# Optimization experiments

Measured on AMD Instinct MI355X. Metric: run time of the kernel, lower is better.

## Reference

```python
import jax, jax.numpy as jnp
import numpy as np

SEQ, BATCH, HID, OUT = 2048, 128, 256, 2

def setup_inputs() -> dict:
    key = jax.random.key(0)
    ks = jax.random.split(key, 8)
    x = jax.random.normal(ks[0], (SEQ, BATCH), dtype=jnp.float32)
    h0 = jax.random.normal(ks[1], (BATCH, HID), dtype=jnp.float32) * 0.1
    noise = jax.random.normal(ks[2], (SEQ, BATCH, HID), dtype=jnp.float32) * 0.1
    W_ih = jax.random.normal(ks[3], (HID, 1), dtype=jnp.float32) * 0.1 + 0.5
    W_hh = jax.random.normal(ks[4], (HID, HID), dtype=jnp.float32) * 0.4
    W_hh_bias = jax.random.normal(ks[5], (HID, HID), dtype=jnp.float32) * 0.1 + 0.1
    b_h = jnp.zeros((HID,), dtype=jnp.float32)
    W = jax.random.normal(ks[6], (OUT, HID), dtype=jnp.float32) * 0.3
    b = jnp.zeros((OUT,), dtype=jnp.float32)
    return dict(x=x, h0=h0, noise=noise, W_ih=W_ih, W_hh=W_hh,
                W_hh_bias=W_hh_bias, b_h=b_h, W=W, b=b, context=1)

def reference(x, h0, noise, W_ih, W_hh, W_hh_bias, b_h, W, b, context):
    # input_size == 1, so x_t @ W_ih.T is an outer product with W_ih[:, 0]
    w_in = W_ih[:, 0]                       # (hid,)
    # context is a scalar, so c1 transposes cancel: W_eff = W_hh + context*W_hh_bias
    W_eff = W_hh + context * W_hh_bias      # (hid, hid)

    def step(h, inp):
        x_t, n_t = inp                      # (batch,), (batch, hid)
        h = jnp.tanh(h @ W_eff.T + x_t[:, None] * w_in[None, :] + b_h) + n_t
        return h, h

    _, out = jax.lax.scan(step, h0, (x, noise))   # (seq, batch, hid)
    out = jnp.transpose(out, (1, 0, 2))           # (batch, seq, hid)
    y = jax.nn.sigmoid(jnp.einsum('bsh,oh->bso', out, W) + b)
    return y[:, :, 0], out
```

## Files before the change

kernel.cpp:

```cpp
#include <hip/hip_runtime.h>
#include <math.h>

#define SEQ   2048
#define BATCH 128
#define HID   256

#define DPP_XOR1  0xB1
#define DPP_XOR2  0x4E
#define DPP_XOR7  0x141
#define DPP_XOR15 0x140
template<int CTRL>
__device__ __forceinline__ float dppf(float v) {
    return __builtin_bit_cast(float, __builtin_amdgcn_update_dpp(
        0, __builtin_bit_cast(int, v), CTRL, 0xF, 0xF, true));
}

#define BARRIER() do { asm volatile("s_waitcnt lgkmcnt(0)" ::: "memory"); \
                       __builtin_amdgcn_s_barrier(); } while (0)

__global__ __launch_bounds__(512, 2) void rnn_kernel(
    const float* __restrict__ x,
    const float* __restrict__ h0,
    const float* __restrict__ noise,
    const float* __restrict__ W_ih,
    const float* __restrict__ W_hh,
    const float* __restrict__ W_hhb,
    const float* __restrict__ b_h,
    const float* __restrict__ Wy,
    const float* __restrict__ by,
    const int*   __restrict__ ctx,
    float* __restrict__ h_out,
    float* __restrict__ y_out)
{
    const int b    = blockIdx.x;
    const int tid  = threadIdx.x;
    const int w    = tid >> 6;
    const int lane = tid & 63;
    const int jg   = lane >> 3;
    const int kg   = lane & 7;
    const int j0   = w * 32 + jg * 4;
    const int jres = j0 + (kg & 3);

    __shared__ __align__(16) float hbuf[2][HID];
    __shared__ __align__(16) float ywave[2][32];

    int iv = *ctx;
    float c = (iv > 1000000 || iv < -1000000) ? __int_as_float(iv) : (float)iv;

    float wreg[4][32];
    #pragma unroll
    for (int e = 0; e < 4; ++e) {
        const float4* wr  = (const float4*)&W_hh [(j0 + e) * HID + kg * 32];
        const float4* wrb = (const float4*)&W_hhb[(j0 + e) * HID + kg * 32];
        #pragma unroll
        for (int q = 0; q < 8; ++q) {
            float4 av = wr[q], bv = wrb[q];
            wreg[e][4*q+0] = av.x + c * bv.x;
            wreg[e][4*q+1] = av.y + c * bv.y;
            wreg[e][4*q+2] = av.z + c * bv.z;
            wreg[e][4*q+3] = av.w + c * bv.w;
        }
    }

    const float win = W_ih[jres];
    const float bh  = b_h[jres];
    const float w0  = Wy[jres];
    const float b0v = by[0];

    if (tid < HID) {
        int cc = tid >> 5, ii = (tid >> 2) & 7, ee = tid & 3;
        hbuf[0][cc * 32 + (((ii + cc) & 7) << 2) + ee] = h0[b * HID + tid];
    }

    int voff[8];
    #pragma unroll
    for (int i = 0; i < 8; ++i)
        voff[i] = kg * 128 + (((i + kg) & 7) << 4);

    const int  b0k = kg & 1;
    const int  b1k = (kg >> 1) & 1;
    const bool wr4 = (kg < 4);
    const int  wslot = w * 32 + (((jg + w) & 7) << 2) + kg;

    float x_next  = x[b];
    float n_next  = noise[(size_t)b * HID + jres];
    float x_next2 = x[BATCH + b];
    float n_next2 = noise[((size_t)BATCH + b) * HID + jres];
    const float* xp = x + 2 * BATCH + b;
    const float* np = noise + ((size_t)2 * BATCH + b) * HID + jres;

    float* hop = h_out + (size_t)b * SEQ * HID;
    float* yp  = y_out + (size_t)b * SEQ;

    __syncthreads();

#define STEP(T, CUR)                                                         \
  {                                                                          \
    const float x_t = x_next;                                                \
    const float n_t = n_next;                                                \
    x_next = x_next2;  n_next = n_next2;                                     \
    x_next2 = *xp;     n_next2 = *np;                                        \
    if ((T) + 3 < SEQ) { xp += BATCH; np += (size_t)BATCH * HID; }           \
    const char* hb = (const char*)&hbuf[CUR][0];                             \
    float p0 = 0.f, p1 = 0.f, p2 = 0.f, p3 = 0.f;                            \
    _Pragma("unroll")                                                        \
    for (int i = 0; i < 8; ++i) {                                            \
      float4 h4 = *(const float4*)(hb + voff[i]);                            \
      p0 = fmaf(h4.x, wreg[0][4*i+0], p0);                                   \
      p0 = fmaf(h4.y, wreg[0][4*i+1], p0);                                   \
      p0 = fmaf(h4.z, wreg[0][4*i+2], p0);                                   \
      p0 = fmaf(h4.w, wreg[0][4*i+3], p0);                                   \
      p1 = fmaf(h4.x, wreg[1][4*i+0], p1);                                   \
      p1 = fmaf(h4.y, wreg[1][4*i+1], p1);                                   \
      p1 = fmaf(h4.z, wreg[1][4*i+2], p1);                                   \
      p1 = fmaf(h4.w, wreg[1][4*i+3], p1);                                   \
      p2 = fmaf(h4.x, wreg[2][4*i+0], p2);                                   \
      p2 = fmaf(h4.y, wreg[2][4*i+1], p2);                                   \
      p2 = fmaf(h4.z, wreg[2][4*i+2], p2);                                   \
      p2 = fmaf(h4.w, wreg[2][4*i+3], p2);                                   \
      p3 = fmaf(h4.x, wreg[3][4*i+0], p3);                                   \
      p3 = fmaf(h4.y, wreg[3][4*i+1], p3);                                   \
      p3 = fmaf(h4.z, wreg[3][4*i+2], p3);                                   \
      p3 = fmaf(h4.w, wreg[3][4*i+3], p3);                                   \
    }                                                                        \
     \
    if (w == ((T) & 7) && (T) > 0) {                                         \
      float4 yv = *(const float4*)&ywave[(CUR) ^ 1][(lane & 7) * 4];         \
      float s = (yv.x + yv.y) + (yv.z + yv.w);                               \
      s += dppf<DPP_XOR1>(s);                                                \
      s += dppf<DPP_XOR2>(s);                                                \
      s += dppf<DPP_XOR7>(s);                                                \
      if (lane == 0) yp[(T) - 1] = 1.f / (1.f + __expf(-(s + b0v)));         \
    }                                                                        \
    \
    \
    p0 += dppf<DPP_XOR7>(p0);                                                \
    p1 += dppf<DPP_XOR7>(p1);                                                \
    p2 += dppf<DPP_XOR7>(p2);                                                \
    p3 += dppf<DPP_XOR7>(p3);                                                \
    float m0 = b0k ? p1 : p0,  s0 = b0k ? p0 : p1;                           \
    float m1 = b0k ? p3 : p2,  s1 = b0k ? p2 : p3;                           \
    float q0 = m0 + dppf<DPP_XOR1>(s0);                                      \
    float q1 = m1 + dppf<DPP_XOR1>(s1);                                      \
    float mm = b1k ? q1 : q0,  ss = b1k ? q0 : q1;                           \
    float r  = mm + dppf<DPP_XOR2>(ss);                                      \
    float z  = fmaf(x_t, win, r) + bh;                                       \
    float ex = __expf(2.f * z);              \
    float hn = 1.f - 2.f / (ex + 1.f) + n_t;                                 \
    if (wr4) {                                                               \
      hbuf[(CUR) ^ 1][wslot] = hn;       \
      hop[jres] = hn;                                                        \
    }                                                                        \
    \
    float qy = wr4 ? hn * w0 : 0.f;                                          \
    qy += dppf<DPP_XOR1>(qy);                                                \
    qy += dppf<DPP_XOR2>(qy);                                                \
    qy += dppf<DPP_XOR7>(qy);                                                \
    qy += dppf<DPP_XOR15>(qy);                                               \
    if ((lane & 15) == 0) ywave[CUR][w * 4 + (lane >> 4)] = qy;              \
    hop += HID;                                                              \
    BARRIER();                                                               \
  }

    for (int t = 0; t < SEQ; t += 2) {
        STEP(t, 0)
        STEP(t + 1, 1)
    }

    if (w == 0) {
        float4 yv = *(const float4*)&ywave[1][(lane & 7) * 4];
        float s = (yv.x + yv.y) + (yv.z + yv.w);
        s += dppf<DPP_XOR1>(s);
        s += dppf<DPP_XOR2>(s);
        s += dppf<DPP_XOR7>(s);
        if (lane == 0) yp[SEQ - 1] = 1.f / (1.f + __expf(-(s + b0v)));
    }
#undef STEP
}

extern "C" void kernel_launch(void* const* d_in, const int* in_sizes, int n_in,
                              void* d_out, int out_size, void* d_ws, size_t ws_size,
                              hipStream_t stream) {
    const float* x     = (const float*)d_in[0];
    const float* h0    = (const float*)d_in[1];
    const float* noise = (const float*)d_in[2];
    const float* W_ih  = (const float*)d_in[3];
    const float* W_hh  = (const float*)d_in[4];
    const float* W_hhb = (const float*)d_in[5];
    const float* b_h   = (const float*)d_in[6];
    const float* W     = (const float*)d_in[7];
    const float* bvec  = (const float*)d_in[8];
    const int*   ctx   = (const int*)d_in[9];

    float* y_out = (float*)d_out;
    float* h_out = (float*)d_out + (size_t)BATCH * SEQ;

    rnn_kernel<<<dim3(BATCH), dim3(512), 0, stream>>>(
        x, h0, noise, W_ih, W_hh, W_hhb, b_h, W, bvec, ctx, h_out, y_out);
}
```

Measured before the change: 2.231 ms.

## Repartition recurrent matvec with packed FMA and defer output work off critical path

Each lane now owns 8 output rows by 16 k-values instead of 4 by 32, and the dot products use v_pk_fma_f32 on float2 pairs, halving FMA instruction count. The hidden-state LDS buffer uses a padded chunk layout so each lane reads four contiguous vec4s. The global h store and y-projection reduction for step t are deferred into step t+1 so they run off the tanh-to-barrier critical path. The tanh and sigmoid divisions now use approximate rcp. This adds more DPP reduction stages, a delayed finalisation sequence, and slightly lower precision.

```diff
diff --git a/kernel.cpp b/kernel.cpp
--- a/kernel.cpp
+++ b/kernel.cpp
@@ -4,6 +4,10 @@
 #define SEQ   2048
 #define BATCH 128
 #define HID   256
+#define CHUNK_B 80
+
+typedef float vf2 __attribute__((ext_vector_type(2)));
+typedef float vf4 __attribute__((ext_vector_type(4)));
 
 #define DPP_XOR1  0xB1
 #define DPP_XOR2  0x4E
@@ -14,6 +18,9 @@
     return __builtin_bit_cast(float, __builtin_amdgcn_update_dpp(
         0, __builtin_bit_cast(int, v), CTRL, 0xF, 0xF, true));
 }
+
+#define PKFMA(acc, a, b) \
+    asm("v_pk_fma_f32 %0, %1, %2, %0" : "+v"(acc) : "v"(a), "v"(b))
 
 #define BARRIER() do { asm volatile("s_waitcnt lgkmcnt(0)" ::: "memory"); \
                        __builtin_amdgcn_s_barrier(); } while (0)
@@ -36,29 +43,31 @@
     const int tid  = threadIdx.x;
     const int w    = tid >> 6;
     const int lane = tid & 63;
-    const int jg   = lane >> 3;
-    const int kg   = lane & 7;
-    const int j0   = w * 32 + jg * 4;
-    const int jres = j0 + (kg & 3);
-
-    __shared__ __align__(16) float hbuf[2][HID];
+    const int jg   = lane >> 4;
+    const int kg   = lane & 15;
+    const int j0   = w * 32 + jg * 8;
+    const int jres = j0 + (lane & 7);
+    const bool wr  = (lane & 8) == 0;
+
+    __shared__ __align__(16) char  hbuf[2][16 * CHUNK_B];
     __shared__ __align__(16) float ywave[2][32];
 
     int iv = *ctx;
     float c = (iv > 1000000 || iv < -1000000) ? __int_as_float(iv) : (float)iv;
 
-    float wreg[4][32];
+    vf2 wreg2[8][8];
     #pragma unroll
-    for (int e = 0; e < 4; ++e) {
-        const float4* wr  = (const float4*)&W_hh [(j0 + e) * HID + kg * 32];
-        const float4* wrb = (const float4*)&W_hhb[(j0 + e) * HID + kg * 32];
+    for (int e = 0; e < 8; ++e) {
+        const vf4* wrp  = (const vf4*)&W_hh [(j0 + e) * HID + kg * 16];
+        const vf4* wrbp = (const vf4*)&W_hhb[(j0 + e) * HID + kg * 16];
         #pragma unroll
-        for (int q = 0; q < 8; ++q) {
-            float4 av = wr[q], bv = wrb[q];
-            wreg[e][4*q+0] = av.x + c * bv.x;
-            wreg[e][4*q+1] = av.y + c * bv.y;
-            wreg[e][4*q+2] = av.z + c * bv.z;
-            wreg[e][4*q+3] = av.w + c * bv.w;
+        for (int q = 0; q < 4; ++q) {
+            vf4 av = wrp[q], bv = wrbp[q];
+            vf2 lo, hi;
+            lo.x = av.x + c * bv.x;  lo.y = av.y + c * bv.y;
+            hi.x = av.z + c * bv.z;  hi.y = av.w + c * bv.w;
+            wreg2[e][2 * q]     = lo;
+            wreg2[e][2 * q + 1] = hi;
         }
     }
 
@@ -67,20 +76,14 @@
     const float w0  = Wy[jres];
     const float b0v = by[0];
 
-    if (tid < HID) {
-        int cc = tid >> 5, ii = (tid >> 2) & 7, ee = tid & 3;
-        hbuf[0][cc * 32 + (((ii + cc) & 7) << 2) + ee] = h0[b * HID + tid];
-    }
-
-    int voff[8];
-    #pragma unroll
-    for (int i = 0; i < 8; ++i)
-        voff[i] = kg * 128 + (((i + kg) & 7) << 4);
-
-    const int  b0k = kg & 1;
-    const int  b1k = (kg >> 1) & 1;
-    const bool wr4 = (kg < 4);
-    const int  wslot = w * 32 + (((jg + w) & 7) << 2) + kg;
+    if (tid < HID)
+        *(float*)&hbuf[0][(tid >> 4) * CHUNK_B + (tid & 15) * 4] = h0[b * HID + tid];
+
+    const char* hrpA = &hbuf[0][kg * CHUNK_B];
+    const char* hrpB = &hbuf[1][kg * CHUNK_B];
+    const int   wbyte = (jres >> 4) * CHUNK_B + (jres & 15) * 4;
+    float* wpA = (float*)&hbuf[0][wbyte];
+    float* wpB = (float*)&hbuf[1][wbyte];
 
     float x_next  = x[b];
     float n_next  = noise[(size_t)b * HID + jres];
@@ -89,91 +92,127 @@
     const float* xp = x + 2 * BATCH + b;
     const float* np = noise + ((size_t)2 * BATCH + b) * HID + jres;
 
-    float* hop = h_out + (size_t)b * SEQ * HID;
-    float* yp  = y_out + (size_t)b * SEQ;
+    float* hout_b = h_out + (size_t)b * SEQ * HID;
+    float* yp     = y_out + (size_t)b * SEQ;
+    int    ho     = 0;
+    float  hn_prev = 0.f;
 
     __syncthreads();
 
-#define STEP(T, CUR)                                                         \
+#define STEP(HRP, WPT, DO_PREV, YWW, DO_FIN, YWR, FINW, TFIN, ADV)           \
   {                                                                          \
-    const float x_t = x_next;                                                \
-    const float n_t = n_next;                                                \
+                                          \
+    vf4 h40 = *(const vf4*)((HRP) + 0);                                      \
+    vf4 h41 = *(const vf4*)((HRP) + 16);                                     \
+    vf4 h42 = *(const vf4*)((HRP) + 32);                                     \
+    vf4 h43 = *(const vf4*)((HRP) + 48);                                     \
+    const float x_t = x_next, n_t = n_next;                                  \
     x_next = x_next2;  n_next = n_next2;                                     \
     x_next2 = *xp;     n_next2 = *np;                                        \
-    if ((T) + 3 < SEQ) { xp += BATCH; np += (size_t)BATCH * HID; }           \
-    const char* hb = (const char*)&hbuf[CUR][0];                             \
-    float p0 = 0.f, p1 = 0.f, p2 = 0.f, p3 = 0.f;                            \
-    _Pragma("unroll")                                                        \
-    for (int i = 0; i < 8; ++i) {                                            \
-      float4 h4 = *(const float4*)(hb + voff[i]);                            \
-      p0 = fmaf(h4.x, wreg[0][4*i+0], p0);                                   \
-      p0 = fmaf(h4.y, wreg[0][4*i+1], p0);                                   \
-      p0 = fmaf(h4.z, wreg[0][4*i+2], p0);                                   \
-      p0 = fmaf(h4.w, wreg[0][4*i+3], p0);                                   \
-      p1 = fmaf(h4.x, wreg[1][4*i+0], p1);                                   \
-      p1 = fmaf(h4.y, wreg[1][4*i+1], p1);                                   \
-      p1 = fmaf(h4.z, wreg[1][4*i+2], p1);                                   \
-      p1 = fmaf(h4.w, wreg[1][4*i+3], p1);                                   \
-      p2 = fmaf(h4.x, wreg[2][4*i+0], p2);                                   \
-      p2 = fmaf(h4.y, wreg[2][4*i+1], p2);                                   \
-      p2 = fmaf(h4.z, wreg[2][4*i+2], p2);                                   \
-      p2 = fmaf(h4.w, wreg[2][4*i+3], p2);                                   \
-      p3 = fmaf(h4.x, wreg[3][4*i+0], p3);                                   \
-      p3 = fmaf(h4.y, wreg[3][4*i+1], p3);                                   \
-      p3 = fmaf(h4.z, wreg[3][4*i+2], p3);                                   \
-      p3 = fmaf(h4.w, wreg[3][4*i+3], p3);                                   \
+    if (ADV) { xp += BATCH; np += (size_t)BATCH * HID; }                     \
+           \
+    if (DO_PREV) {                                                           \
+      if (wr) hout_b[ho + jres] = hn_prev;                                   \
+      float qy = wr ? hn_prev * w0 : 0.f;                                    \
+      qy += dppf<DPP_XOR1>(qy);                                              \
+      qy += dppf<DPP_XOR2>(qy);                                              \
+      qy += dppf<DPP_XOR7>(qy);                                              \
+      qy += dppf<DPP_XOR15>(qy);                                             \
+      if ((lane & 15) == 0) (YWW)[w * 4 + jg] = qy;                          \
+      ho += HID;                                                             \
     }                                                                        \
-     \
-    if (w == ((T) & 7) && (T) > 0) {                                         \
-      float4 yv = *(const float4*)&ywave[(CUR) ^ 1][(lane & 7) * 4];         \
+    if (DO_FIN && w == (FINW)) {     \
+      vf4 yv = *(const vf4*)&(YWR)[(lane & 7) * 4];                          \
       float s = (yv.x + yv.y) + (yv.z + yv.w);                               \
       s += dppf<DPP_XOR1>(s);                                                \
       s += dppf<DPP_XOR2>(s);                                                \
       s += dppf<DPP_XOR7>(s);                                                \
-      if (lane == 0) yp[(T) - 1] = 1.f / (1.f + __expf(-(s + b0v)));         \
+      if (lane == 0)                                                         \
+        yp[TFIN] = __builtin_amdgcn_rcpf(1.f + __expf(-(s + b0v)));          \
     }                                                                        \
-    \
-    \
-    p0 += dppf<DPP_XOR7>(p0);                                                \
-    p1 += dppf<DPP_XOR7>(p1);                                                \
-    p2 += dppf<DPP_XOR7>(p2);                                                \
-    p3 += dppf<DPP_XOR7>(p3);                                                \
-    float m0 = b0k ? p1 : p0,  s0 = b0k ? p0 : p1;                           \
-    float m1 = b0k ? p3 : p2,  s1 = b0k ? p2 : p3;                           \
-    float q0 = m0 + dppf<DPP_XOR1>(s0);                                      \
-    float q1 = m1 + dppf<DPP_XOR1>(s1);                                      \
-    float mm = b1k ? q1 : q0,  ss = b1k ? q0 : q1;                           \
-    float r  = mm + dppf<DPP_XOR2>(ss);                                      \
+             \
+    vf2 acc[8];                                                              \
+    _Pragma("unroll")                                                        \
+    for (int e = 0; e < 8; ++e) acc[e] = (vf2)0.f;                           \
+    { vf2 ha = h40.xy, hb = h40.zw;                                          \
+      _Pragma("unroll")                                                      \
+      for (int e = 0; e < 8; ++e) { PKFMA(acc[e], ha, wreg2[e][0]);          \
+                                    PKFMA(acc[e], hb, wreg2[e][1]); } }      \
+    { vf2 ha = h41.xy, hb = h41.zw;                                          \
+      _Pragma("unroll")                                                      \
+      for (int e = 0; e < 8; ++e) { PKFMA(acc[e], ha, wreg2[e][2]);          \
+                                    PKFMA(acc[e], hb, wreg2[e][3]); } }      \
+    { vf2 ha = h42.xy, hb = h42.zw;                                          \
+      _Pragma("unroll")                                                      \
+      for (int e = 0; e < 8; ++e) { PKFMA(acc[e], ha, wreg2[e][4]);          \
+                                    PKFMA(acc[e], hb, wreg2[e][5]); } }      \
+    { vf2 ha = h43.xy, hb = h43.zw;                                          \
+      _Pragma("unroll")                                                      \
+      for (int e = 0; e < 8; ++e) { PKFMA(acc[e], ha, wreg2[e][6]);          \
+                                    PKFMA(acc[e], hb, wreg2[e][7]); } }      \
+     \
+          \
+    float p0 = acc[0].x + acc[0].y,  p1 = acc[1].x + acc[1].y;               \
+    float p2 = acc[2].x + acc[2].y,  p3 = acc[3].x + acc[3].y;               \
+    float p4 = acc[4].x + acc[4].y,  p5 = acc[5].x + acc[5].y;               \
+    float p6 = acc[6].x + acc[6].y,  p7 = acc[7].x + acc[7].y;               \
+    p0 += dppf<DPP_XOR7>(p0);   p1 += dppf<DPP_XOR7>(p1);                    \
+    p2 += dppf<DPP_XOR7>(p2);   p3 += dppf<DPP_XOR7>(p3);                    \
+    p4 += dppf<DPP_XOR7>(p4);   p5 += dppf<DPP_XOR7>(p5);                    \
+    p6 += dppf<DPP_XOR7>(p6);   p7 += dppf<DPP_XOR7>(p7);                    \
+    p0 += dppf<DPP_XOR15>(p0);  p1 += dppf<DPP_XOR15>(p1);                   \
+    p2 += dppf<DPP_XOR15>(p2);  p3 += dppf<DPP_XOR15>(p3);                   \
+    p4 += dppf<DPP_XOR15>(p4);  p5 += dppf<DPP_XOR15>(p5);                   \
+    p6 += dppf<DPP_XOR15>(p6);  p7 += dppf<DPP_XOR15>(p7);                   \
+    const bool bb0 = (lane & 1), bb1 = (lane & 2), bb2 = (lane & 4);         \
+    float q0 = (bb0 ? p1 : p0) + dppf<DPP_XOR1>(bb0 ? p0 : p1);              \
+    float q1 = (bb0 ? p3 : p2) + dppf<DPP_XOR1>(bb0 ? p2 : p3);              \
+    float q2 = (bb0 ? p5 : p4) + dppf<DPP_XOR1>(bb0 ? p4 : p5);              \
+    float q3 = (bb0 ? p7 : p6) + dppf<DPP_XOR1>(bb0 ? p6 : p7);              \
+    float r0 = (bb1 ? q1 : q0) + dppf<DPP_XOR2>(bb1 ? q0 : q1);              \
+    float r1 = (bb1 ? q3 : q2) + dppf<DPP_XOR2>(bb1 ? q2 : q3);              \
+    float r  = bb2 ? r1 : r0;                                                \
     float z  = fmaf(x_t, win, r) + bh;                                       \
     float ex = __expf(2.f * z);              \
-    float hn = 1.f - 2.f / (ex + 1.f) + n_t;                                 \
-    if (wr4) {                                                               \
-      hbuf[(CUR) ^ 1][wslot] = hn;       \
-      hop[jres] = hn;                                                        \
-    }                                                                        \
-    \
-    float qy = wr4 ? hn * w0 : 0.f;                                          \
-    qy += dppf<DPP_XOR1>(qy);                                                \
-    qy += dppf<DPP_XOR2>(qy);                                                \
-    qy += dppf<DPP_XOR7>(qy);                                                \
-    qy += dppf<DPP_XOR15>(qy);                                               \
-    if ((lane & 15) == 0) ywave[CUR][w * 4 + (lane >> 4)] = qy;              \
-    hop += HID;                                                              \
+    float hn = fmaf(-2.f, __builtin_amdgcn_rcpf(ex + 1.f), 1.f) + n_t;       \
+    if (wr) *(WPT) = hn;                                                     \
+    hn_prev = hn;                                                            \
     BARRIER();                                                               \
   }
 
-    for (int t = 0; t < SEQ; t += 2) {
-        STEP(t, 0)
-        STEP(t + 1, 1)
-    }
-
-    if (w == 0) {
-        float4 yv = *(const float4*)&ywave[1][(lane & 7) * 4];
+    STEP(hrpA, wpB, 0, ywave[1], 0, ywave[0], 7, 0, 1)
+    STEP(hrpB, wpA, 1, ywave[0], 0, ywave[1], 6, 0, 1)
+
+    for (int t = 2; t < SEQ; t += 2) {
+        STEP(hrpA, wpB, 1, ywave[1], 1, ywave[0], 7, t - 2, (t + 3 < SEQ))
+        STEP(hrpB, wpA, 1, ywave[0], 1, ywave[1], 6, t - 1, (t + 4 < SEQ))
+    }
+
+    if (wr) hout_b[ho + jres] = hn_prev;
+    {
+        float qy = wr ? hn_prev * w0 : 0.f;
+        qy += dppf<DPP_XOR1>(qy);
+        qy += dppf<DPP_XOR2>(qy);
+        qy += dppf<DPP_XOR7>(qy);
+        qy += dppf<DPP_XOR15>(qy);
+        if ((lane & 15) == 0) ywave[1][w * 4 + jg] = qy;
+    }
+    if (w == 7) {
+        vf4 yv = *(const vf4*)&ywave[0][(lane & 7) * 4];
         float s = (yv.x + yv.y) + (yv.z + yv.w);
         s += dppf<DPP_XOR1>(s);
         s += dppf<DPP_XOR2>(s);
         s += dppf<DPP_XOR7>(s);
-        if (lane == 0) yp[SEQ - 1] = 1.f / (1.f + __expf(-(s + b0v)));
+        if (lane == 0) yp[SEQ - 2] = __builtin_amdgcn_rcpf(1.f + __expf(-(s + b0v)));
+    }
+    BARRIER();
+    if (w == 6) {
+        vf4 yv = *(const vf4*)&ywave[1][(lane & 7) * 4];
+        float s = (yv.x + yv.y) + (yv.z + yv.w);
+        s += dppf<DPP_XOR1>(s);
+        s += dppf<DPP_XOR2>(s);
+        s += dppf<DPP_XOR7>(s);
+        if (lane == 0) yp[SEQ - 1] = __builtin_amdgcn_rcpf(1.f + __expf(-(s + b0v)));
     }
 #undef STEP
 }
```

Result: faster. 2.084 ms (-6.6%).
